# Performance work log

Hardware: AMD Instinct MI355X
Metric: run time of the kernel (lower is better)

Reference implementation:

```python
import jax, jax.numpy as jnp
import numpy as np

B, L, D, H, MEM, POL = 32, 256, 768, 12, 384, 3
DK = D // H
ALPHA, BETA, GAMA = 1.0, 0.25, 0.1


def _forward(sequence_output, pooled_output, adj_reshape, src_mask, aspect_mask,
             ln_g, ln_b, wq, bq, wk, bk, wd, bd, weight_m, bias_m,
             wa0, ba0, wa1, ba1, ws0, bs0, ws1, bs1, affine1, affine2, wc, bc):
    b, l, d = sequence_output.shape
    h = weight_m.shape[0]
    dk = d // h

    # custom LayerNorm (torch std is unbiased, ddof=1)
    mu = sequence_output.mean(-1, keepdims=True)
    sd = jnp.std(sequence_output, axis=-1, keepdims=True, ddof=1)
    x = ln_g * (sequence_output - mu) / (sd + 1e-6) + ln_b  # gcn_inputs (dropout = eval identity)

    aspect_outs = x * aspect_mask[:, :, None]

    # multi-head projections  [B,H,L,dk]
    q = (x @ wq + bq).reshape(b, l, h, dk).transpose(0, 2, 1, 3)
    k = (x @ wk + bk).reshape(b, l, h, dk).transpose(0, 2, 1, 3)
    asp = aspect_outs @ wd + bd                       # [B,L,dk]
    asp = jnp.broadcast_to(asp[:, None], (b, h, l, dk))

    # aspect-conditioned scores: tanh(aspect @ W_m @ K^T + b_m)   [B,H,L,L]
    asps = jnp.tanh(jnp.einsum('bhld,hde,bhme->bhlm', asp, weight_m, k) + bias_m[0])
    avg = asps.sum(axis=-2) / l                       # [B,H,L]

    # fusion overwrite: for each aspect index idx, row idx and col idx <- avg.
    # Sequential loop semantics (ascending idx, row-then-col) collapse to:
    #   both aspect (i,j): value = avg[min(i,j)];  row-only: avg[j];  col-only: avg[i]
    is_asp = aspect_mask > 0                          # [B,L]
    rowm = is_asp[:, None, :, None]
    colm = is_asp[:, None, None, :]
    avg_i = avg[..., :, None]                         # [B,H,L,1]
    avg_j = avg[..., None, :]                         # [B,H,1,L]
    ge = (jnp.arange(l)[:, None] >= jnp.arange(l)[None, :])  # i>=j -> min=j
    both_val = jnp.where(ge, avg_j, avg_i)
    aspect_scores = jnp.where(rowm & colm, both_val,
                      jnp.where(rowm, avg_j,
                        jnp.where(colm, avg_i, asps)))

    # standard scaled-dot attention
    scores = jnp.einsum('bhld,bhmd->bhlm', q, k) / jnp.sqrt(jnp.float32(dk))
    scores = jnp.where(src_mask[:, None, None, :] == 0, -1e9, scores)
    s_attn = jax.nn.softmax(scores, axis=-1)          # dropout = eval identity

    aspect_score_avg = aspect_scores.mean(axis=1)     # [B,L,L]
    adj_s = s_attn.mean(axis=1)                       # [B,L,L]

    eye = jnp.eye(l, dtype=adj_s.dtype)
    adj_s = adj_s * (1.0 - eye) + eye                 # zero diag then add identity
    adj_s = src_mask[:, :, None] * adj_s

    adj_r = jnp.exp(ALPHA * adj_reshape)
    dist_mask = aspect_score_avg > BETA
    adj_r = jnp.where(dist_mask, 1.0, adj_r)
    adj_ag = adj_r * aspect_score_avg

    log_p = jax.nn.log_softmax(adj_ag, axis=-1)
    log_q = jax.nn.log_softmax(adj_s, axis=-1)
    q_t = jnp.exp(log_q)
    kl = jnp.sum(q_t * (log_q - log_p))
    kl_loss = jnp.exp(-1.0 * kl * GAMA)

    denom_s = adj_s.sum(axis=2, keepdims=True) + 1.0
    denom_ag = adj_ag.sum(axis=2, keepdims=True) + 1.0

    out_ag, out_s = x, x
    was = [(wa0, ba0), (wa1, ba1)]
    wss = [(ws0, bs0), (ws1, bs1)]
    for li in range(2):
        g_ag = jax.nn.relu(((adj_ag @ out_ag) @ was[li][0] + was[li][1]) / denom_ag)
        g_s = jax.nn.relu(((adj_s @ out_s) @ wss[li][0] + wss[li][1]) / denom_s)
        A1 = jax.nn.softmax(jnp.einsum('bld,de,bme->blm', g_ag, affine1, g_s), axis=-1)
        A2 = jax.nn.softmax(jnp.einsum('bld,de,bme->blm', g_s, affine2, g_ag), axis=-1)
        out_ag = A1 @ g_s
        out_s = A2 @ g_ag   # gcn_drop = eval identity

    asp_wn = aspect_mask.sum(axis=1, keepdims=True)   # [B,1]
    m = aspect_mask[:, :, None]
    outputs1 = (out_ag * m).sum(axis=1) / asp_wn      # [B,MEM]
    outputs2 = (out_s * m).sum(axis=1) / asp_wn

    final = jnp.concatenate([outputs1, outputs2, pooled_output], axis=-1) @ wc + bc
    return final, kl_loss


def setup_inputs() -> dict:
    key = jax.random.key(0)
    ks = jax.random.split(key, 16)
    s = 0.02
    pos = jnp.arange(L)
    start = 5 + (jnp.arange(B) % 16)
    aspect_mask = ((pos[None, :] >= start[:, None]) & (pos[None, :] < start[:, None] + 3)).astype(jnp.float32)
    f32 = jnp.float32
    return {
        'sequence_output': jax.random.normal(ks[0], (B, L, D), f32),
        'pooled_output': jax.random.normal(ks[1], (B, D), f32),
        'adj_reshape': jax.random.uniform(ks[2], (B, L, L), f32),
        'src_mask': jnp.ones((B, L), f32),
        'aspect_mask': aspect_mask,
        'ln_g': jnp.ones((D,), f32), 'ln_b': jnp.zeros((D,), f32),
        'wq': jax.random.normal(ks[3], (D, D), f32) * s, 'bq': jnp.zeros((D,), f32),
        'wk': jax.random.normal(ks[4], (D, D), f32) * s, 'bk': jnp.zeros((D,), f32),
        'wd': jax.random.normal(ks[5], (D, DK), f32) * s, 'bd': jnp.zeros((DK,), f32),
        'weight_m': jax.random.normal(ks[6], (H, DK, DK), f32) * s,
        'bias_m': jnp.zeros((1,), f32),
        'wa0': jax.random.normal(ks[7], (D, MEM), f32) * s, 'ba0': jnp.zeros((MEM,), f32),
        'wa1': jax.random.normal(ks[8], (MEM, MEM), f32) * s, 'ba1': jnp.zeros((MEM,), f32),
        'ws0': jax.random.normal(ks[9], (D, MEM), f32) * s, 'bs0': jnp.zeros((MEM,), f32),
        'ws1': jax.random.normal(ks[10], (MEM, MEM), f32) * s, 'bs1': jnp.zeros((MEM,), f32),
        'affine1': jax.random.normal(ks[11], (MEM, MEM), f32) * s,
        'affine2': jax.random.normal(ks[12], (MEM, MEM), f32) * s,
        'wc': jax.random.normal(ks[13], (2 * D, POL), f32) * s, 'bc': jnp.zeros((POL,), f32),
    }


def reference(sequence_output, pooled_output, adj_reshape, src_mask, aspect_mask,
              ln_g, ln_b, wq, bq, wk, bk, wd, bd, weight_m, bias_m,
              wa0, ba0, wa1, ba1, ws0, bs0, ws1, bs1, affine1, affine2, wc, bc):
    return _forward(sequence_output, pooled_output, adj_reshape, src_mask, aspect_mask,
                    ln_g, ln_b, wq, bq, wk, bk, wd, bd, weight_m, bias_m,
                    wa0, ba0, wa1, ba1, ws0, bs0, ws1, bs1, affine1, affine2, wc, bc)
```

## Files before the change

### kernel.cpp

```cpp
#include <hip/hip_runtime.h>

#define B_ 32
#define L_ 256
#define D_ 768
#define H_ 12
#define DK_ 64
#define MEM_ 384

typedef __attribute__((ext_vector_type(8))) short bfrag8;
typedef __attribute__((ext_vector_type(8))) unsigned short us8;
typedef __attribute__((ext_vector_type(4))) float f32x4;

__device__ inline unsigned short f2bf(float f) {
  unsigned u = __float_as_uint(f);
  return (unsigned short)((u + 0x7fffu + ((u >> 16) & 1u)) >> 16);
}
__device__ inline float bf2f(unsigned short u) {
  return __uint_as_float(((unsigned)u) << 16);
}
__device__ inline float tanh_fast(float x) {
  x = fminf(fmaxf(x, -30.f), 30.f);
  float e = __expf(2.f * x);
  return (e - 1.f) * __builtin_amdgcn_rcpf(e + 1.f);
}
__device__ inline void gload_lds16(const unsigned short* g, unsigned short* l) {
  __builtin_amdgcn_global_load_lds(
      (__attribute__((address_space(1))) void*)(g),
      (__attribute__((address_space(3))) void*)(l), 16, 0, 0);
}

__device__ inline float waveRedSum(float v) {
#pragma unroll
  for (int o = 32; o; o >>= 1) v += __shfl_xor(v, o, 64);
  return v;
}
__device__ inline float waveRedMax(float v) {
#pragma unroll
  for (int o = 32; o; o >>= 1) v = fmaxf(v, __shfl_xor(v, o, 64));
  return v;
}
__device__ inline float blkRedSum(float v, float* red) {
  v = waveRedSum(v);
  int w = threadIdx.x >> 6;
  __syncthreads();
  if ((threadIdx.x & 63) == 0) red[w] = v;
  __syncthreads();
  return red[0] + red[1] + red[2] + red[3];
}
__device__ inline float blkRedMax(float v, float* red) {
  v = waveRedMax(v);
  int w = threadIdx.x >> 6;
  __syncthreads();
  if ((threadIdx.x & 63) == 0) red[w] = v;
  __syncthreads();
  return fmaxf(fmaxf(red[0], red[1]), fmaxf(red[2], red[3]));
}

__global__ __launch_bounds__(256) void prep_kernel(
    const float* __restrict__ seq, const float* __restrict__ lng,
    const float* __restrict__ lnb, float* __restrict__ xout,
    unsigned short* __restrict__ xbf,
    const float* __restrict__ wq, unsigned short* __restrict__ wqT,
    const float* __restrict__ wk, unsigned short* __restrict__ wkT,
    const float* __restrict__ wa0, unsigned short* __restrict__ wa0T,
    const float* __restrict__ ws0, unsigned short* __restrict__ ws0T,
    const float* __restrict__ wa1, unsigned short* __restrict__ wa1T,
    const float* __restrict__ ws1, unsigned short* __restrict__ ws1T,
    const float* __restrict__ aff1, unsigned short* __restrict__ aff1T,
    const float* __restrict__ aff2, unsigned short* __restrict__ aff2T,
    const float* __restrict__ wd, unsigned short* __restrict__ wdT,
    const float* __restrict__ wm, unsigned short* __restrict__ wmT) {
  int bid = blockIdx.x;
  if (bid >= 600) {
    long row = bid - 600;
    const float* p = seq + row * D_;
    float v[3];
#pragma unroll
    for (int i = 0; i < 3; ++i) v[i] = p[threadIdx.x + i * 256];
    __shared__ float red[4];
    float s = v[0] + v[1] + v[2];
    s = blkRedSum(s, red);
    float mu = s * (1.f / D_);
    float ss = 0.f;
#pragma unroll
    for (int i = 0; i < 3; ++i) { float d = v[i] - mu; ss += d * d; }
    ss = blkRedSum(ss, red);
    float sd = sqrtf(ss * (1.f / (D_ - 1)));
    float inv = 1.f / (sd + 1e-6f);
#pragma unroll
    for (int i = 0; i < 3; ++i) {
      int c = threadIdx.x + i * 256;
      float o = lng[c] * (v[i] - mu) * inv + lnb[c];
      xout[row * D_ + c] = o;
      xbf[row * D_ + c] = f2bf(o);
    }
    return;
  }
  const float* src; unsigned short* dst; int Rr, Cc, tIdx;
  if (bid < 144)      { src = wq;   dst = wqT;   Rr = 768; Cc = 768; tIdx = bid; }
  else if (bid < 288) { src = wk;   dst = wkT;   Rr = 768; Cc = 768; tIdx = bid - 144; }
  else if (bid < 360) { src = wa0;  dst = wa0T;  Rr = 768; Cc = 384; tIdx = bid - 288; }
  else if (bid < 432) { src = ws0;  dst = ws0T;  Rr = 768; Cc = 384; tIdx = bid - 360; }
  else if (bid < 468) { src = wa1;  dst = wa1T;  Rr = 384; Cc = 384; tIdx = bid - 432; }
  else if (bid < 504) { src = ws1;  dst = ws1T;  Rr = 384; Cc = 384; tIdx = bid - 468; }
  else if (bid < 540) { src = aff1; dst = aff1T; Rr = 384; Cc = 384; tIdx = bid - 504; }
  else if (bid < 576) { src = aff2; dst = aff2T; Rr = 384; Cc = 384; tIdx = bid - 540; }
  else if (bid < 588) { src = wd;   dst = wdT;   Rr = 768; Cc = 64;  tIdx = bid - 576; }
  else { int h = bid - 588; src = wm + h * 4096; dst = wmT + h * 4096; Rr = 64; Cc = 64; tIdx = 0; }
  __shared__ float tile[64][65];
  int nx = Cc >> 6;
  int c0 = (tIdx % nx) * 64, r0 = (tIdx / nx) * 64;
  int tx = threadIdx.x & 63, ty = threadIdx.x >> 6;
#pragma unroll
  for (int i = 0; i < 16; ++i)
    tile[ty + i * 4][tx] = src[(long)(r0 + ty + i * 4) * Cc + c0 + tx];
  __syncthreads();
#pragma unroll
  for (int i = 0; i < 16; ++i)
    dst[(long)(c0 + ty + i * 4) * Rr + r0 + tx] = f2bf(tile[tx][ty + i * 4]);
}

template <int MR>
__global__ __launch_bounds__(256) void gemm_bb(
    const unsigned short* __restrict__ A, const unsigned short* __restrict__ Bt,
    float* __restrict__ C, unsigned short* __restrict__ Cbf,
    unsigned short* __restrict__ CT,
    int M, int N, int K, long sA, long sB, long sC, long sCT,
    const float* __restrict__ bias, const float* __restrict__ rowDiv, int relu,
    const unsigned short* __restrict__ A2, const unsigned short* __restrict__ Bt2,
    float* __restrict__ C2, unsigned short* __restrict__ Cbf2,
    unsigned short* __restrict__ CT2,
    const float* __restrict__ bias2, const float* __restrict__ rowDiv2, int zsplit) {
  constexpr int MFRAG = MR / 32;
  constexpr int RW = MR / 2;
  constexpr int ASH = MR * 32;
  constexpr int BUFS = ASH + 4096;
  constexpr int TSH = 64 * (MR + 8);
  constexpr int SMN = (2 * BUFS > TSH) ? 2 * BUFS : TSH;
  __shared__ alignas(16) unsigned short smem[SMN];
  const int tid = threadIdx.x;
  const int bn = blockIdx.x, bm = blockIdx.y;
  int bz = blockIdx.z;
  const unsigned short* Ap = A; const unsigned short* Btp = Bt;
  float* Cp = C; unsigned short* Cbp = Cbf; unsigned short* CTp = CT;
  const float* biasp = bias; const float* rowDivp = rowDiv;
  if (zsplit > 0 && bz >= zsplit) {
    bz -= zsplit;
    Ap = A2; Btp = Bt2; Cp = C2; Cbp = Cbf2; CTp = CT2; biasp = bias2; rowDivp = rowDiv2;
  }
  Ap += (long)bz * sA; Btp += (long)bz * sB;
  if (Cp) Cp += (long)bz * sC;
  if (Cbp) Cbp += (long)bz * sC;
  if (CTp) CTp += (long)bz * sCT;

  f32x4 acc[MFRAG][4] = {};
  const int l = tid & 63, w = tid >> 6;
  const int wr = w >> 1, wc = w & 1;
  const int lr = l & 15, sg = l >> 4;

  const int rc = l >> 2;
  const int sslot = (l & 3) ^ ((rc >> 1) & 3);
  const unsigned short* gA0 = Ap + (long)(bm * MR + w * 16 + rc) * K + sslot * 8;
  const unsigned short* gA1 = (MR == 128)
      ? Ap + (long)(bm * MR + (w + 4) * 16 + rc) * K + sslot * 8 : nullptr;
  const unsigned short* gB0 = Btp + (long)(bn * 128 + w * 16 + rc) * K + sslot * 8;
  const unsigned short* gB1 = Btp + (long)(bn * 128 + (w + 4) * 16 + rc) * K + sslot * 8;
  const int stA0 = w * 512, stA1 = (w + 4) * 512;
  const int stB0 = ASH + w * 512, stB1 = ASH + (w + 4) * 512;

  const int swz = (sg ^ ((lr >> 1) & 3)) * 8;
  int aoff[MFRAG], boff[4];
#pragma unroll
  for (int m = 0; m < MFRAG; ++m) aoff[m] = (wr * RW + m * 16 + lr) * 32 + swz;
#pragma unroll
  for (int n = 0; n < 4; ++n) boff[n] = ASH + (wc * 64 + n * 16 + lr) * 32 + swz;

  const int nt = K >> 5;
  gload_lds16(gA0, smem + stA0);
  if (MR == 128) gload_lds16(gA1, smem + stA1);
  gload_lds16(gB0, smem + stB0);
  gload_lds16(gB1, smem + stB1);
  __syncthreads();

  for (int t = 0; t < nt; ++t) {
    const int cur = (t & 1) * BUFS;
    if (t + 1 < nt) {
      const int nxt = ((t + 1) & 1) * BUFS;
      const int k1 = (t + 1) << 5;
      gload_lds16(gA0 + k1, smem + nxt + stA0);
      if (MR == 128) gload_lds16(gA1 + k1, smem + nxt + stA1);
      gload_lds16(gB0 + k1, smem + nxt + stB0);
      gload_lds16(gB1 + k1, smem + nxt + stB1);
    }
    bfrag8 af[MFRAG], bf[4];
#pragma unroll
    for (int m = 0; m < MFRAG; ++m) af[m] = *(const bfrag8*)(smem + cur + aoff[m]);
#pragma unroll
    for (int n = 0; n < 4; ++n) bf[n] = *(const bfrag8*)(smem + cur + boff[n]);
#pragma unroll
    for (int m = 0; m < MFRAG; ++m)
#pragma unroll
      for (int n = 0; n < 4; ++n)
        acc[m][n] = __builtin_amdgcn_mfma_f32_16x16x32_bf16(af[m], bf[n], acc[m][n], 0, 0, 0);
    __syncthreads();
  }

  if (Cp || Cbp) {
#pragma unroll
    for (int m = 0; m < MFRAG; ++m) {
#pragma unroll
      for (int r = 0; r < 4; ++r) {
        int row = bm * MR + wr * RW + m * 16 + (l >> 4) * 4 + r;
        float rd = rowDivp ? 1.f / rowDivp[(long)bz * M + row] : 1.f;
#pragma unroll
        for (int n = 0; n < 4; ++n) {
          int col = bn * 128 + wc * 64 + n * 16 + lr;
          float v = acc[m][n][r];
          if (biasp) v += biasp[col];
          v *= rd;
          if (relu) v = fmaxf(v, 0.f);
          if (Cp) Cp[(long)row * N + col] = v;
          if (Cbp) Cbp[(long)row * N + col] = f2bf(v);
        }
      }
    }
  }
  if (CT) {
    auto Ts = (unsigned short(*)[MR + 8])smem;
#pragma unroll
    for (int ch = 0; ch < 2; ++ch) {
      __syncthreads();
      if (wc == ch) {
#pragma unroll
        for (int m = 0; m < MFRAG; ++m) {
#pragma unroll
          for (int r = 0; r < 4; ++r) {
            int rowl = wr * RW + m * 16 + (l >> 4) * 4 + r;
            float rd = rowDivp ? 1.f / rowDivp[(long)bz * M + bm * MR + rowl] : 1.f;
#pragma unroll
            for (int n = 0; n < 4; ++n) {
              int col = bn * 128 + wc * 64 + n * 16 + lr;
              float v = acc[m][n][r];
              if (biasp) v += biasp[col];
              v *= rd;
              if (relu) v = fmaxf(v, 0.f);
              Ts[n * 16 + lr][rowl] = f2bf(v);
            }
          }
        }
      }
      __syncthreads();
      int trow = tid >> 2, tc = (tid & 3) * (MR / 4);
      int colg = bn * 128 + ch * 64 + trow;
      int rowg = bm * MR + tc;
      unsigned short* dp = CTp + (long)(rowg >> 8) * sCT + (long)colg * 256 + (rowg & 255);
#pragma unroll
      for (int j = 0; j < MR / 32; ++j)
        *(us8*)(dp + j * 8) = *(const us8*)&Ts[trow][tc + j * 8];
    }
  }
}

__global__ __launch_bounds__(256) void attn_asp(
    const unsigned short* __restrict__ qbf, const unsigned short* __restrict__ kbf,
    const float* __restrict__ srcm, float* __restrict__ adj_s,
    unsigned short* __restrict__ adjsbf,
    const unsigned short* __restrict__ xbf, const unsigned short* __restrict__ wdT,
    const float* __restrict__ amask, const float* __restrict__ bd,
    unsigned short* __restrict__ aspbf) {
  int t = threadIdx.x;
  int w = t >> 6, l = t & 63;
  int lr = l & 15, kg = (l >> 4) * 8;
  if (blockIdx.x >= 512) {
    int l0 = (blockIdx.x - 512) << 4;
    const unsigned short* ap = xbf + (long)(l0 + lr) * D_ + kg;
    const unsigned short* bp = wdT + (long)(w * 16 + lr) * D_ + kg;
    f32x4 acc = {};
#pragma unroll
    for (int k0 = 0; k0 < D_; k0 += 32) {
      bfrag8 af = *(const bfrag8*)(ap + k0);
      bfrag8 bf = *(const bfrag8*)(bp + k0);
      acc = __builtin_amdgcn_mfma_f32_16x16x32_bf16(af, bf, acc, 0, 0, 0);
    }
    int col = w * 16 + lr;
#pragma unroll
    for (int r = 0; r < 4; ++r) {
      int row = l0 + (l >> 4) * 4 + r;
      float v = acc[r] * amask[row] + bd[col];
      aspbf[(long)row * DK_ + col] = f2bf(v);
    }
    return;
  }
  int blk = blockIdx.x;
  int b = blk >> 4, l0 = (blk & 15) << 4;
  int rbase = (l >> 4) * 4;
  __shared__ float red[6][2][16][8];
  float acc[4][4] = {};
  float cmv[4];
#pragma unroll
  for (int ct = 0; ct < 4; ++ct) cmv[ct] = srcm[b * L_ + w * 64 + ct * 16 + lr];

#pragma unroll 1
  for (int hp = 0; hp < 6; ++hp) {
    const unsigned short* ap = qbf + ((long)b * L_ + l0 + lr) * D_ + hp * 128 + kg;
    bfrag8 a00 = *(const bfrag8*)ap;
    bfrag8 a01 = *(const bfrag8*)(ap + 32);
    bfrag8 a10 = *(const bfrag8*)(ap + 64);
    bfrag8 a11 = *(const bfrag8*)(ap + 96);
    bfrag8 kv[4][4];
#pragma unroll
    for (int ct = 0; ct < 4; ++ct) {
      const unsigned short* bp =
          kbf + ((long)b * L_ + w * 64 + ct * 16 + lr) * D_ + hp * 128 + kg;
      kv[ct][0] = *(const bfrag8*)bp;
      kv[ct][1] = *(const bfrag8*)(bp + 32);
      kv[ct][2] = *(const bfrag8*)(bp + 64);
      kv[ct][3] = *(const bfrag8*)(bp + 96);
    }
    float sv0[4][4], sv1[4][4];
#pragma unroll
    for (int ct = 0; ct < 4; ++ct) {
      f32x4 c0 = {}, c1 = {};
      c0 = __builtin_amdgcn_mfma_f32_16x16x32_bf16(a00, kv[ct][0], c0, 0, 0, 0);
      c0 = __builtin_amdgcn_mfma_f32_16x16x32_bf16(a01, kv[ct][1], c0, 0, 0, 0);
      c1 = __builtin_amdgcn_mfma_f32_16x16x32_bf16(a10, kv[ct][2], c1, 0, 0, 0);
      c1 = __builtin_amdgcn_mfma_f32_16x16x32_bf16(a11, kv[ct][3], c1, 0, 0, 0);
      bool msk = (cmv[ct] == 0.f);
#pragma unroll
      for (int r = 0; r < 4; ++r) {
        sv0[ct][r] = msk ? -1e9f : c0[r] * 0.125f;
        sv1[ct][r] = msk ? -1e9f : c1[r] * 0.125f;
      }
    }
    float mx0a[4], mx1a[4];
#pragma unroll
    for (int r = 0; r < 4; ++r) {
      float m0 = fmaxf(fmaxf(sv0[0][r], sv0[1][r]), fmaxf(sv0[2][r], sv0[3][r]));
      float m1 = fmaxf(fmaxf(sv1[0][r], sv1[1][r]), fmaxf(sv1[2][r], sv1[3][r]));
#pragma unroll
      for (int o = 1; o < 16; o <<= 1) {
        m0 = fmaxf(m0, __shfl_xor(m0, o, 64));
        m1 = fmaxf(m1, __shfl_xor(m1, o, 64));
      }
      mx0a[r] = m0; mx1a[r] = m1;
      float s0 = 0.f, s1 = 0.f;
#pragma unroll
      for (int ct = 0; ct < 4; ++ct) {
        float e0 = __expf(sv0[ct][r] - m0);
        float e1 = __expf(sv1[ct][r] - m1);
        sv0[ct][r] = e0; sv1[ct][r] = e1;
        s0 += e0; s1 += e1;
      }
#pragma unroll
      for (int o = 1; o < 16; o <<= 1) {
        s0 += __shfl_xor(s0, o, 64);
        s1 += __shfl_xor(s1, o, 64);
      }
      if (lr == 0) {
        red[hp][0][rbase + r][w] = m0;
        red[hp][0][rbase + r][4 + w] = s0;
        red[hp][1][rbase + r][w] = m1;
        red[hp][1][rbase + r][4 + w] = s1;
      }
    }
    __syncthreads();
#pragma unroll
    for (int r = 0; r < 4; ++r) {
      f32x4 m4 = *(const f32x4*)&red[hp][0][rbase + r][0];
      f32x4 s4 = *(const f32x4*)&red[hp][0][rbase + r][4];
      float mt = fmaxf(fmaxf(m4[0], m4[1]), fmaxf(m4[2], m4[3]));
      float tot = s4[0] * __expf(m4[0] - mt) + s4[1] * __expf(m4[1] - mt) +
                  s4[2] * __expf(m4[2] - mt) + s4[3] * __expf(m4[3] - mt);
      float sc0 = __expf(mx0a[r] - mt) * __builtin_amdgcn_rcpf(tot);
      f32x4 n4 = *(const f32x4*)&red[hp][1][rbase + r][0];
      f32x4 t4 = *(const f32x4*)&red[hp][1][rbase + r][4];
      float nt = fmaxf(fmaxf(n4[0], n4[1]), fmaxf(n4[2], n4[3]));
      float tt = t4[0] * __expf(n4[0] - nt) + t4[1] * __expf(n4[1] - nt) +
                 t4[2] * __expf(n4[2] - nt) + t4[3] * __expf(n4[3] - nt);
      float sc1 = __expf(mx1a[r] - nt) * __builtin_amdgcn_rcpf(tt);
#pragma unroll
      for (int ct = 0; ct < 4; ++ct)
        acc[ct][r] += sv0[ct][r] * sc0 + sv1[ct][r] * sc1;
    }
  }

#pragma unroll
  for (int r = 0; r < 4; ++r) {
    int row = l0 + rbase + r;
    float rm = srcm[b * L_ + row];
#pragma unroll
    for (int ct = 0; ct < 4; ++ct) {
      int col = w * 64 + ct * 16 + lr;
      float v = acc[ct][r] * (1.f / H_);
      if (col == row) v = 1.f;
      v *= rm;
      long idx = ((long)b * L_ + row) * L_ + col;
      adj_s[idx] = v;
      adjsbf[idx] = f2bf(v);
    }
  }
}

__global__ __launch_bounds__(256) void asp_wm_v2(const unsigned short* __restrict__ aspbf,
                                                 const unsigned short* __restrict__ wmT,
                                                 unsigned short* __restrict__ tmpA) {
  int bh = blockIdx.x;
  int b = bh / H_, h = bh % H_;
  int t = threadIdx.x;
  int w = t >> 6, l = t & 63;
  int lr = l & 15, kg = (l >> 4) * 8;
  const unsigned short* wp = wmT + h * 4096;
  f32x4 acc[4][4] = {};
#pragma unroll
  for (int ks = 0; ks < 2; ++ks) {
    int k0 = ks * 32;
    bfrag8 af[4], bf[4];
#pragma unroll
    for (int m = 0; m < 4; ++m)
      af[m] = *(const bfrag8*)(aspbf + (long)(b * L_ + w * 64 + m * 16 + lr) * DK_ + k0 + kg);
#pragma unroll
    for (int n = 0; n < 4; ++n)
      bf[n] = *(const bfrag8*)(wp + (n * 16 + lr) * 64 + k0 + kg);
#pragma unroll
    for (int m = 0; m < 4; ++m)
#pragma unroll
      for (int n = 0; n < 4; ++n)
        acc[m][n] = __builtin_amdgcn_mfma_f32_16x16x32_bf16(af[m], bf[n], acc[m][n], 0, 0, 0);
  }
#pragma unroll
  for (int m = 0; m < 4; ++m)
#pragma unroll
    for (int n = 0; n < 4; ++n)
#pragma unroll
      for (int r = 0; r < 4; ++r) {
        int row = w * 64 + m * 16 + (l >> 4) * 4 + r;
        int col = n * 16 + lr;
        tmpA[(((long)b * H_ + h) * L_ + row) * DK_ + col] = f2bf(acc[m][n][r]);
      }
}

__global__ __launch_bounds__(256) void gemm_sfmx(
    const unsigned short* __restrict__ u1, const unsigned short* __restrict__ g1,
    unsigned short* __restrict__ P1,
    const unsigned short* __restrict__ u2, const unsigned short* __restrict__ g2,
    unsigned short* __restrict__ P2) {
  int bm = blockIdx.x;
  int bz = blockIdx.y;
  const unsigned short* Ap; const unsigned short* Bp; unsigned short* Pp;
  if (bz < 32) {
    Ap = u1 + (long)bz * L_ * MEM_; Bp = g1 + (long)bz * L_ * MEM_;
    Pp = P1 + (long)bz * L_ * L_;
  } else {
    int z = bz - 32;
    Ap = u2 + (long)z * L_ * MEM_; Bp = g2 + (long)z * L_ * MEM_;
    Pp = P2 + (long)z * L_ * L_;
  }
  __shared__ unsigned short As[64][40];
  __shared__ unsigned short Bs[256][40];
  __shared__ float redm[2][64];
  __shared__ float reds[2][64];
  const int t = threadIdx.x;
  const int l = t & 63, w = t >> 6;
  const int wr = w >> 1, wc = w & 1;
  const int lr = l & 15, kg = (l >> 4) * 8;
  f32x4 acc[2][8] = {};
  const int arA = t >> 2, akA = (t & 3) * 8;

  for (int k0 = 0; k0 < MEM_; k0 += 32) {
    *(us8*)&As[arA][akA] = *(const us8*)(Ap + (long)(bm * 64 + arA) * MEM_ + k0 + akA);
#pragma unroll
    for (int j = 0; j < 4; ++j)
      *(us8*)&Bs[t][j * 8] = *(const us8*)(Bp + (long)t * MEM_ + k0 + j * 8);
    __syncthreads();
    bfrag8 af[2], bf[8];
#pragma unroll
    for (int m = 0; m < 2; ++m) af[m] = *(const bfrag8*)&As[wr * 32 + m * 16 + lr][kg];
#pragma unroll
    for (int n = 0; n < 8; ++n) bf[n] = *(const bfrag8*)&Bs[wc * 128 + n * 16 + lr][kg];
#pragma unroll
    for (int m = 0; m < 2; ++m)
#pragma unroll
      for (int n = 0; n < 8; ++n)
        acc[m][n] = __builtin_amdgcn_mfma_f32_16x16x32_bf16(af[m], bf[n], acc[m][n], 0, 0, 0);
    __syncthreads();
  }

#pragma unroll
  for (int m = 0; m < 2; ++m) {
#pragma unroll
    for (int r = 0; r < 4; ++r) {
      int lrow = wr * 32 + m * 16 + (l >> 4) * 4 + r;
      float mx = -1e30f;
#pragma unroll
      for (int n = 0; n < 8; ++n) mx = fmaxf(mx, acc[m][n][r]);
#pragma unroll
      for (int o = 1; o < 16; o <<= 1) mx = fmaxf(mx, __shfl_xor(mx, o, 64));
      if (lr == 0) redm[wc][lrow] = mx;
    }
  }
  __syncthreads();
#pragma unroll
  for (int m = 0; m < 2; ++m) {
#pragma unroll
    for (int r = 0; r < 4; ++r) {
      int lrow = wr * 32 + m * 16 + (l >> 4) * 4 + r;
      float mx = fmaxf(redm[0][lrow], redm[1][lrow]);
      float s = 0.f;
#pragma unroll
      for (int n = 0; n < 8; ++n) {
        float e = __expf(acc[m][n][r] - mx);
        acc[m][n][r] = e;
        s += e;
      }
#pragma unroll
      for (int o = 1; o < 16; o <<= 1) s += __shfl_xor(s, o, 64);
      if (lr == 0) reds[wc][lrow] = s;
    }
  }
  __syncthreads();
#pragma unroll
  for (int m = 0; m < 2; ++m) {
#pragma unroll
    for (int r = 0; r < 4; ++r) {
      int lrow = wr * 32 + m * 16 + (l >> 4) * 4 + r;
      float inv = 1.f / (reds[0][lrow] + reds[1][lrow]);
      int row = bm * 64 + lrow;
#pragma unroll
      for (int n = 0; n < 8; ++n) {
        int col = wc * 128 + n * 16 + lr;
        Pp[(long)row * L_ + col] = f2bf(acc[m][n][r] * inv);
      }
    }
  }
}

__global__ __launch_bounds__(256) void asps_mean_v2(
    const unsigned short* __restrict__ tmpA,
    const unsigned short* __restrict__ kbf,
    const float* __restrict__ bias_m,
    float* __restrict__ asps_mean) {
  int blk = blockIdx.x;
  int b = blk >> 4, l0 = (blk & 15) << 4;
  int t = threadIdx.x;
  int w = t >> 6, l = t & 63;
  int lr = l & 15, kg = (l >> 4) * 8;
  float bm = bias_m[0];
  float accg[4][4] = {};
  for (int h = 0; h < H_; ++h) {
    const unsigned short* ap = tmpA + (((long)b * H_ + h) * L_ + l0 + lr) * 64 + kg;
    bfrag8 af0 = *(const bfrag8*)ap;
    bfrag8 af1 = *(const bfrag8*)(ap + 32);
#pragma unroll
    for (int ct = 0; ct < 4; ++ct) {
      const unsigned short* bp =
          kbf + ((long)b * L_ + w * 64 + ct * 16 + lr) * D_ + h * 64 + kg;
      bfrag8 bf0 = *(const bfrag8*)bp;
      bfrag8 bf1 = *(const bfrag8*)(bp + 32);
      f32x4 accl = {};
      accl = __builtin_amdgcn_mfma_f32_16x16x32_bf16(af0, bf0, accl, 0, 0, 0);
      accl = __builtin_amdgcn_mfma_f32_16x16x32_bf16(af1, bf1, accl, 0, 0, 0);
#pragma unroll
      for (int r = 0; r < 4; ++r) accg[ct][r] += tanh_fast(accl[r] + bm);
    }
  }
#pragma unroll
  for (int ct = 0; ct < 4; ++ct) {
    int col = w * 64 + ct * 16 + lr;
#pragma unroll
    for (int r = 0; r < 4; ++r) {
      int row = l0 + (l >> 4) * 4 + r;
      asps_mean[((long)b * L_ + row) * L_ + col] = accg[ct][r] * (1.f / H_);
    }
  }
}

__global__ __launch_bounds__(1024) void avgh_kernel(const float* __restrict__ asps_mean,
                                                    float* __restrict__ avgH) {
  int b = blockIdx.x;
  int m = threadIdx.x & 255, q = threadIdx.x >> 8;
  __shared__ float part[4][256];
  float s = 0.f;
  for (int l = q * 64; l < q * 64 + 64; ++l)
    s += asps_mean[((long)b * L_ + l) * L_ + m];
  part[q][m] = s;
  __syncthreads();
  if (q == 0)
    avgH[b * L_ + m] = (part[0][m] + part[1][m] + part[2][m] + part[3][m]) * (1.f / L_);
}

__global__ __launch_bounds__(256) void adjag_kl(const float* __restrict__ asps_mean,
                                                const float* __restrict__ avgH,
                                                const float* __restrict__ amask,
                                                const float* __restrict__ adjr,
                                                const float* __restrict__ adj_s,
                                                float* __restrict__ adj_ag,
                                                unsigned short* __restrict__ adjagbf,
                                                float* __restrict__ klpart,
                                                float* __restrict__ den_s,
                                                float* __restrict__ den_ag) {
  long row = blockIdx.x;
  int m = threadIdx.x;
  int l = (int)(row & 255);
  int b = (int)(row >> 8);
  long idx = row * L_ + m;
  bool rowa = amask[b * L_ + l] > 0.f;
  bool cola = amask[b * L_ + m] > 0.f;
  float asa;
  if (rowa && cola) asa = (l >= m) ? avgH[b * L_ + m] : avgH[b * L_ + l];
  else if (rowa)    asa = avgH[b * L_ + m];
  else if (cola)    asa = avgH[b * L_ + l];
  else              asa = asps_mean[idx];
  float r = (asa > 0.25f) ? 1.f : expf(adjr[idx]);
  float a = r * asa;
  adj_ag[idx] = a;
  adjagbf[idx] = f2bf(a);

  __shared__ float red[4];
  float s = adj_s[idx];
  float sum_s = blkRedSum(s, red);
  float sum_a = blkRedSum(a, red);
  float mx_s = blkRedMax(s, red);
  float mx_a = blkRedMax(a, red);
  float es = expf(s - mx_s), ea = expf(a - mx_a);
  float ses = blkRedSum(es, red);
  float sea = blkRedSum(ea, red);
  float logq = (s - mx_s) - logf(ses);
  float logp = (a - mx_a) - logf(sea);
  float term = (es / ses) * (logq - logp);
  float kp = blkRedSum(term, red);
  if (m == 0) {
    klpart[row] = kp;
    den_s[row] = sum_s + 1.f;
    den_ag[row] = sum_a + 1.f;
  }
}

__global__ __launch_bounds__(256) void final_kernel(const unsigned short* __restrict__ o_ag,
                                                    const unsigned short* __restrict__ o_s,
                                                    const float* __restrict__ pooled,
                                                    const float* __restrict__ amask,
                                                    const float* __restrict__ wc,
                                                    const float* __restrict__ bc,
                                                    const float* __restrict__ klpart,
                                                    float* __restrict__ dout) {
  int b = blockIdx.x, t = threadIdx.x;
  __shared__ float red[4];
  if (b == B_) {
    float s = 0.f;
    for (int i = t; i < B_ * L_; i += 256) s += klpart[i];
    s = blkRedSum(s, red);
    if (t == 0) dout[96] = expf(-s * 0.1f);
    return;
  }
  __shared__ float cS[1536];
  __shared__ float maskS[256];
  maskS[t] = amask[b * L_ + t];
  float wn = blkRedSum(maskS[t], red);
  for (int e = t; e < MEM_; e += 256) {
    float s1 = 0.f, s2 = 0.f;
    for (int l = 0; l < L_; ++l) {
      float mk = maskS[l];
      if (mk != 0.f) {
        s1 += mk * bf2f(o_ag[((long)b * L_ + l) * MEM_ + e]);
        s2 += mk * bf2f(o_s[((long)b * L_ + l) * MEM_ + e]);
      }
    }
    cS[e] = s1 / wn;
    cS[MEM_ + e] = s2 / wn;
  }
  for (int j = t; j < D_; j += 256) cS[2 * MEM_ + j] = pooled[b * D_ + j];
  __syncthreads();
  float p0 = 0.f, p1 = 0.f, p2 = 0.f;
  for (int j = t; j < 1536; j += 256) {
    float v = cS[j];
    p0 += v * wc[j * 3 + 0];
    p1 += v * wc[j * 3 + 1];
    p2 += v * wc[j * 3 + 2];
  }
  p0 = blkRedSum(p0, red);
  p1 = blkRedSum(p1, red);
  p2 = blkRedSum(p2, red);
  if (t == 0) {
    dout[b * 3 + 0] = p0 + bc[0];
    dout[b * 3 + 1] = p1 + bc[1];
    dout[b * 3 + 2] = p2 + bc[2];
  }
}

extern "C" void kernel_launch(void* const* d_in, const int* in_sizes, int n_in,
                              void* d_out, int out_size, void* d_ws, size_t ws_size,
                              hipStream_t stream) {
  const float* seq    = (const float*)d_in[0];
  const float* pooled = (const float*)d_in[1];
  const float* adjr   = (const float*)d_in[2];
  const float* srcm   = (const float*)d_in[3];
  const float* amask  = (const float*)d_in[4];
  const float* ln_g   = (const float*)d_in[5];
  const float* ln_b   = (const float*)d_in[6];
  const float* wq     = (const float*)d_in[7];
  const float* bq     = (const float*)d_in[8];
  const float* wk     = (const float*)d_in[9];
  const float* bk     = (const float*)d_in[10];
  const float* wd     = (const float*)d_in[11];
  const float* bd     = (const float*)d_in[12];
  const float* wm     = (const float*)d_in[13];
  const float* bm     = (const float*)d_in[14];
  const float* wa0    = (const float*)d_in[15];
  const float* ba0    = (const float*)d_in[16];
  const float* wa1    = (const float*)d_in[17];
  const float* ba1    = (const float*)d_in[18];
  const float* ws0    = (const float*)d_in[19];
  const float* bs0    = (const float*)d_in[20];
  const float* ws1    = (const float*)d_in[21];
  const float* bs1    = (const float*)d_in[22];
  const float* aff1   = (const float*)d_in[23];
  const float* aff2   = (const float*)d_in[24];
  const float* wc     = (const float*)d_in[25];
  const float* bc     = (const float*)d_in[26];

  float* ws = (float*)d_ws;
  float* S0 = ws;
  float* S1 = S0 + 6291456;
  float* S2 = S1 + 3145728;
  float* S3 = S2 + 3145728;
  float* S4 = S3 + 3145728;
  float* S5 = S4 + 524288;
  float* adj_s  = S5 + 2097152;
  float* adj_ag = adj_s + 2097152;
  unsigned short* adjsbf  = (unsigned short*)(adj_ag + 2097152);
  unsigned short* adjagbf = adjsbf + 2097152;
  unsigned short* wT      = adjagbf + 2097152;
  unsigned short* wqT   = wT;
  unsigned short* wkT   = wT + 589824;
  unsigned short* wa0T  = wT + 1179648;
  unsigned short* ws0T  = wT + 1474560;
  unsigned short* wa1T  = wT + 1769472;
  unsigned short* ws1T  = wT + 1916928;
  unsigned short* aff1T = wT + 2064384;
  unsigned short* aff2T = wT + 2211840;
  float* tail   = (float*)(wT + 2359296);
  float* avgH   = tail;
  float* den_s  = avgH + 8192;
  float* den_ag = den_s + 8192;
  float* klp    = den_ag + 8192;

  float* x = S0;
  unsigned short* o_agbf = (unsigned short*)S0;
  unsigned short* o_sbf  = o_agbf + 3145728;
  unsigned short* gTag   = o_agbf + 6291456;
  unsigned short* gTs    = o_agbf + 9437184;
  unsigned short* xbf    = (unsigned short*)S1;
  unsigned short* qbf    = (unsigned short*)S2;
  unsigned short* tmpA   = (unsigned short*)S2;
  unsigned short* g_agbf = (unsigned short*)S2;
  unsigned short* g_sbf  = g_agbf + 3145728;
  unsigned short* kbf    = (unsigned short*)S3;
  unsigned short* tTag   = (unsigned short*)S3;
  unsigned short* tTs    = tTag + 3145728;
  unsigned short* u1bf   = (unsigned short*)S3;
  unsigned short* u2bf   = u1bf + 3145728;
  unsigned short* aspbf  = (unsigned short*)S4;
  unsigned short* wdT    = aspbf + 524288;
  unsigned short* wmT    = wdT + 49152;
  float* asps = S5;
  unsigned short* P1bf = (unsigned short*)S5;
  unsigned short* P2bf = P1bf + 2097152;
  float* dout = (float*)d_out;

  const long sAdjSh = (long)L_ * L_;
  const long sMemSh = (long)L_ * MEM_;

  prep_kernel<<<600 + B_ * L_, 256, 0, stream>>>(
      seq, ln_g, ln_b, x, xbf, wq, wqT, wk, wkT, wa0, wa0T, ws0, ws0T,
      wa1, wa1T, ws1, ws1T, aff1, aff1T, aff2, aff2T, wd, wdT, wm, wmT);
  gemm_bb<128><<<dim3(6, 64, 2), 256, 0, stream>>>(
      xbf, wqT, nullptr, qbf, nullptr, 8192, 768, 768, 0, 0, 0, 0, bq, nullptr, 0,
      xbf, wkT, nullptr, kbf, nullptr, bk, nullptr, 1);
  attn_asp<<<1024, 256, 0, stream>>>(qbf, kbf, srcm, adj_s, adjsbf,
                                     xbf, wdT, amask, bd, aspbf);
  asp_wm_v2<<<B_ * H_, 256, 0, stream>>>(aspbf, wmT, tmpA);
  asps_mean_v2<<<B_ * 16, 256, 0, stream>>>(tmpA, kbf, bm, asps);
  avgh_kernel<<<B_, 1024, 0, stream>>>(asps, avgH);
  adjag_kl<<<B_ * L_, 256, 0, stream>>>(asps, avgH, amask, adjr, adj_s,
                                        adj_ag, adjagbf, klp, den_s, den_ag);

  for (int li = 0; li < 2; ++li) {
    int Kd = li ? MEM_ : D_;
    const unsigned short* inag = li ? o_agbf : xbf;
    const unsigned short* ins  = li ? o_sbf : xbf;
    const unsigned short* wAT = li ? wa1T : wa0T;
    const float* bA = li ? ba1 : ba0;
    const unsigned short* wST = li ? ws1T : ws0T;
    const float* bS = li ? bs1 : bs0;
    gemm_bb<64><<<dim3(3, 128, 2), 256, 0, stream>>>(
        inag, wAT, nullptr, nullptr, tTag, 8192, MEM_, Kd, 0, 0, 0, sMemSh,
        nullptr, nullptr, 0,
        ins, wST, nullptr, nullptr, tTs, nullptr, nullptr, 1);
    gemm_bb<64><<<dim3(3, 4, 64), 256, 0, stream>>>(
        adjagbf, tTag, nullptr, g_agbf, gTag, L_, MEM_, L_, sAdjSh, sMemSh, sMemSh,
        sMemSh, bA, den_ag, 1,
        adjsbf, tTs, nullptr, g_sbf, gTs, bS, den_s, 32);
    gemm_bb<64><<<dim3(3, 128, 2), 256, 0, stream>>>(
        g_agbf, aff1T, nullptr, u1bf, nullptr, 8192, MEM_, MEM_, 0, 0, 0, 0,
        nullptr, nullptr, 0,
        g_sbf, aff2T, nullptr, u2bf, nullptr, nullptr, nullptr, 1);
    gemm_sfmx<<<dim3(4, 64), 256, 0, stream>>>(u1bf, g_sbf, P1bf, u2bf, g_agbf, P2bf);
    gemm_bb<64><<<dim3(3, 4, 64), 256, 0, stream>>>(
        P1bf, gTs, nullptr, o_agbf, nullptr, L_, MEM_, L_, sAdjSh, sMemSh, sMemSh, 0,
        nullptr, nullptr, 0,
        P2bf, gTag, nullptr, o_sbf, nullptr, nullptr, nullptr, 32);
  }

  final_kernel<<<B_ + 1, 256, 0, stream>>>(o_agbf, o_sbf, pooled, amask, wc, bc,
                                           klp, dout);
}
```

Before: 408.0 us.

## Split attention heads across two blocks, defer adj_s finalize, async double-buffer gemm_sfmx

The attention kernel now splits the six head-pairs across two blocks per row tile, doubling the grid. Each block writes fp32 partial sums, and the blocks are interleaved so that neighbouring blocks work on different batches. The diagonal, mask and bf16 conversion of adj_s move into adjag_kl, which sums the two partials there, and the unused fp32 adj_s and adj_ag stores are dropped. gemm_sfmx switches to direct global-to-LDS loads into swizzled, double-buffered shared memory so the next tile's loads overlap the current tile's MFMAs. In exchange, the extra fp32 partial buffers add write and read traffic.

```diff
diff --git a/kernel.cpp b/kernel.cpp
--- a/kernel.cpp
+++ b/kernel.cpp
@@ -263,16 +263,16 @@
 
 __global__ __launch_bounds__(256) void attn_asp(
     const unsigned short* __restrict__ qbf, const unsigned short* __restrict__ kbf,
-    const float* __restrict__ srcm, float* __restrict__ adj_s,
-    unsigned short* __restrict__ adjsbf,
+    const float* __restrict__ srcm,
+    float* __restrict__ part0, float* __restrict__ part1,
     const unsigned short* __restrict__ xbf, const unsigned short* __restrict__ wdT,
     const float* __restrict__ amask, const float* __restrict__ bd,
     unsigned short* __restrict__ aspbf) {
   int t = threadIdx.x;
   int w = t >> 6, l = t & 63;
   int lr = l & 15, kg = (l >> 4) * 8;
-  if (blockIdx.x >= 512) {
-    int l0 = (blockIdx.x - 512) << 4;
+  if (blockIdx.x >= 1024) {
+    int l0 = (blockIdx.x - 1024) << 4;
     const unsigned short* ap = xbf + (long)(l0 + lr) * D_ + kg;
     const unsigned short* bp = wdT + (long)(w * 16 + lr) * D_ + kg;
     f32x4 acc = {};
@@ -291,17 +291,21 @@
     }
     return;
   }
-  int blk = blockIdx.x;
-  int b = blk >> 4, l0 = (blk & 15) << 4;
+  int d = blockIdx.x;
+  int b = (d & 7) + 8 * ((d >> 3) & 3);
+  int rest = d >> 5;
+  int l0 = (rest & 15) << 4;
+  int half = rest >> 4;
   int rbase = (l >> 4) * 4;
-  __shared__ float red[6][2][16][8];
+  __shared__ float red[3][2][16][8];
   float acc[4][4] = {};
   float cmv[4];
 #pragma unroll
   for (int ct = 0; ct < 4; ++ct) cmv[ct] = srcm[b * L_ + w * 64 + ct * 16 + lr];
 
 #pragma unroll 1
-  for (int hp = 0; hp < 6; ++hp) {
+  for (int ph = 0; ph < 3; ++ph) {
+    int hp = half * 3 + ph;
     const unsigned short* ap = qbf + ((long)b * L_ + l0 + lr) * D_ + hp * 128 + kg;
     bfrag8 a00 = *(const bfrag8*)ap;
     bfrag8 a01 = *(const bfrag8*)(ap + 32);
@@ -357,23 +361,23 @@
         s1 += __shfl_xor(s1, o, 64);
       }
       if (lr == 0) {
-        red[hp][0][rbase + r][w] = m0;
-        red[hp][0][rbase + r][4 + w] = s0;
-        red[hp][1][rbase + r][w] = m1;
-        red[hp][1][rbase + r][4 + w] = s1;
+        red[ph][0][rbase + r][w] = m0;
+        red[ph][0][rbase + r][4 + w] = s0;
+        red[ph][1][rbase + r][w] = m1;
+        red[ph][1][rbase + r][4 + w] = s1;
       }
     }
     __syncthreads();
 #pragma unroll
     for (int r = 0; r < 4; ++r) {
-      f32x4 m4 = *(const f32x4*)&red[hp][0][rbase + r][0];
-      f32x4 s4 = *(const f32x4*)&red[hp][0][rbase + r][4];
+      f32x4 m4 = *(const f32x4*)&red[ph][0][rbase + r][0];
+      f32x4 s4 = *(const f32x4*)&red[ph][0][rbase + r][4];
       float mt = fmaxf(fmaxf(m4[0], m4[1]), fmaxf(m4[2], m4[3]));
       float tot = s4[0] * __expf(m4[0] - mt) + s4[1] * __expf(m4[1] - mt) +
                   s4[2] * __expf(m4[2] - mt) + s4[3] * __expf(m4[3] - mt);
       float sc0 = __expf(mx0a[r] - mt) * __builtin_amdgcn_rcpf(tot);
-      f32x4 n4 = *(const f32x4*)&red[hp][1][rbase + r][0];
-      f32x4 t4 = *(const f32x4*)&red[hp][1][rbase + r][4];
+      f32x4 n4 = *(const f32x4*)&red[ph][1][rbase + r][0];
+      f32x4 t4 = *(const f32x4*)&red[ph][1][rbase + r][4];
       float nt = fmaxf(fmaxf(n4[0], n4[1]), fmaxf(n4[2], n4[3]));
       float tt = t4[0] * __expf(n4[0] - nt) + t4[1] * __expf(n4[1] - nt) +
                  t4[2] * __expf(n4[2] - nt) + t4[3] * __expf(n4[3] - nt);
@@ -384,19 +388,14 @@
     }
   }
 
+  float* pp = half ? part1 : part0;
 #pragma unroll
   for (int r = 0; r < 4; ++r) {
     int row = l0 + rbase + r;
-    float rm = srcm[b * L_ + row];
 #pragma unroll
     for (int ct = 0; ct < 4; ++ct) {
       int col = w * 64 + ct * 16 + lr;
-      float v = acc[ct][r] * (1.f / H_);
-      if (col == row) v = 1.f;
-      v *= rm;
-      long idx = ((long)b * L_ + row) * L_ + col;
-      adj_s[idx] = v;
-      adjsbf[idx] = f2bf(v);
+      pp[((long)b * L_ + row) * L_ + col] = acc[ct][r];
     }
   }
 }
@@ -444,6 +443,11 @@
     unsigned short* __restrict__ P1,
     const unsigned short* __restrict__ u2, const unsigned short* __restrict__ g2,
     unsigned short* __restrict__ P2) {
+  constexpr int ASH = 64 * 32;
+  constexpr int BUFS = ASH + 8192;
+  __shared__ alignas(16) unsigned short smem[2 * BUFS];
+  __shared__ float redm[2][64];
+  __shared__ float reds[2][64];
   int bm = blockIdx.x;
   int bz = blockIdx.y;
   const unsigned short* Ap; const unsigned short* Bp; unsigned short* Pp;
@@ -455,28 +459,51 @@
     Ap = u2 + (long)z * L_ * MEM_; Bp = g2 + (long)z * L_ * MEM_;
     Pp = P2 + (long)z * L_ * L_;
   }
-  __shared__ unsigned short As[64][40];
-  __shared__ unsigned short Bs[256][40];
-  __shared__ float redm[2][64];
-  __shared__ float reds[2][64];
   const int t = threadIdx.x;
   const int l = t & 63, w = t >> 6;
   const int wr = w >> 1, wc = w & 1;
-  const int lr = l & 15, kg = (l >> 4) * 8;
+  const int lr = l & 15, sg = l >> 4;
   f32x4 acc[2][8] = {};
-  const int arA = t >> 2, akA = (t & 3) * 8;
-
-  for (int k0 = 0; k0 < MEM_; k0 += 32) {
-    *(us8*)&As[arA][akA] = *(const us8*)(Ap + (long)(bm * 64 + arA) * MEM_ + k0 + akA);
-#pragma unroll
-    for (int j = 0; j < 4; ++j)
-      *(us8*)&Bs[t][j * 8] = *(const us8*)(Bp + (long)t * MEM_ + k0 + j * 8);
-    __syncthreads();
+
+  const int rc = l >> 2;
+  const int sslot = (l & 3) ^ ((rc >> 1) & 3);
+  const unsigned short* gA = Ap + (long)(bm * 64 + w * 16 + rc) * MEM_ + sslot * 8;
+  const unsigned short* gB[4];
+#pragma unroll
+  for (int j = 0; j < 4; ++j)
+    gB[j] = Bp + (long)(w * 64 + j * 16 + rc) * MEM_ + sslot * 8;
+  const int stA = w * 512;
+  int stB[4];
+#pragma unroll
+  for (int j = 0; j < 4; ++j) stB[j] = ASH + (w * 4 + j) * 512;
+
+  const int swz = (sg ^ ((lr >> 1) & 3)) * 8;
+  int aoff[2], boff[8];
+#pragma unroll
+  for (int m = 0; m < 2; ++m) aoff[m] = (wr * 32 + m * 16 + lr) * 32 + swz;
+#pragma unroll
+  for (int n = 0; n < 8; ++n) boff[n] = ASH + (wc * 128 + n * 16 + lr) * 32 + swz;
+
+  gload_lds16(gA, smem + stA);
+#pragma unroll
+  for (int j = 0; j < 4; ++j) gload_lds16(gB[j], smem + stB[j]);
+  __syncthreads();
+
+  constexpr int NT = MEM_ / 32;
+  for (int tt = 0; tt < NT; ++tt) {
+    const int cur = (tt & 1) * BUFS;
+    if (tt + 1 < NT) {
+      const int nxt = ((tt + 1) & 1) * BUFS;
+      const int k1 = (tt + 1) << 5;
+      gload_lds16(gA + k1, smem + nxt + stA);
+#pragma unroll
+      for (int j = 0; j < 4; ++j) gload_lds16(gB[j] + k1, smem + nxt + stB[j]);
+    }
     bfrag8 af[2], bf[8];
 #pragma unroll
-    for (int m = 0; m < 2; ++m) af[m] = *(const bfrag8*)&As[wr * 32 + m * 16 + lr][kg];
-#pragma unroll
-    for (int n = 0; n < 8; ++n) bf[n] = *(const bfrag8*)&Bs[wc * 128 + n * 16 + lr][kg];
+    for (int m = 0; m < 2; ++m) af[m] = *(const bfrag8*)(smem + cur + aoff[m]);
+#pragma unroll
+    for (int n = 0; n < 8; ++n) bf[n] = *(const bfrag8*)(smem + cur + boff[n]);
 #pragma unroll
     for (int m = 0; m < 2; ++m)
 #pragma unroll
@@ -588,12 +615,14 @@
     avgH[b * L_ + m] = (part[0][m] + part[1][m] + part[2][m] + part[3][m]) * (1.f / L_);
 }
 
-__global__ __launch_bounds__(256) void adjag_kl(const float* __restrict__ asps_mean,
+__global__ __launch_bounds__(256) void adjag_kl(const float* __restrict__ part0,
+                                                const float* __restrict__ part1,
+                                                const float* __restrict__ srcm,
+                                                const float* __restrict__ asps_mean,
                                                 const float* __restrict__ avgH,
                                                 const float* __restrict__ amask,
                                                 const float* __restrict__ adjr,
-                                                const float* __restrict__ adj_s,
-                                                float* __restrict__ adj_ag,
+                                                unsigned short* __restrict__ adjsbf,
                                                 unsigned short* __restrict__ adjagbf,
                                                 float* __restrict__ klpart,
                                                 float* __restrict__ den_s,
@@ -603,6 +632,10 @@
   int l = (int)(row & 255);
   int b = (int)(row >> 8);
   long idx = row * L_ + m;
+  float s = (part0[idx] + part1[idx]) * (1.f / H_);
+  if (m == l) s = 1.f;
+  s *= srcm[b * L_ + l];
+  adjsbf[idx] = f2bf(s);
   bool rowa = amask[b * L_ + l] > 0.f;
   bool cola = amask[b * L_ + m] > 0.f;
   float asa;
@@ -612,11 +645,9 @@
   else              asa = asps_mean[idx];
   float r = (asa > 0.25f) ? 1.f : expf(adjr[idx]);
   float a = r * asa;
-  adj_ag[idx] = a;
   adjagbf[idx] = f2bf(a);
 
   __shared__ float red[4];
-  float s = adj_s[idx];
   float sum_s = blkRedSum(s, red);
   float sum_a = blkRedSum(a, red);
   float mx_s = blkRedMax(s, red);
@@ -725,9 +756,9 @@
   float* S3 = S2 + 3145728;
   float* S4 = S3 + 3145728;
   float* S5 = S4 + 524288;
-  float* adj_s  = S5 + 2097152;
-  float* adj_ag = adj_s + 2097152;
-  unsigned short* adjsbf  = (unsigned short*)(adj_ag + 2097152);
+  float* part0  = S5 + 2097152;
+  float* part1  = part0 + 2097152;
+  unsigned short* adjsbf  = (unsigned short*)(part1 + 2097152);
   unsigned short* adjagbf = adjsbf + 2097152;
   unsigned short* wT      = adjagbf + 2097152;
   unsigned short* wqT   = wT;
@@ -776,13 +807,13 @@
   gemm_bb<128><<<dim3(6, 64, 2), 256, 0, stream>>>(
       xbf, wqT, nullptr, qbf, nullptr, 8192, 768, 768, 0, 0, 0, 0, bq, nullptr, 0,
       xbf, wkT, nullptr, kbf, nullptr, bk, nullptr, 1);
-  attn_asp<<<1024, 256, 0, stream>>>(qbf, kbf, srcm, adj_s, adjsbf,
+  attn_asp<<<1536, 256, 0, stream>>>(qbf, kbf, srcm, part0, part1,
                                      xbf, wdT, amask, bd, aspbf);
   asp_wm_v2<<<B_ * H_, 256, 0, stream>>>(aspbf, wmT, tmpA);
   asps_mean_v2<<<B_ * 16, 256, 0, stream>>>(tmpA, kbf, bm, asps);
   avgh_kernel<<<B_, 1024, 0, stream>>>(asps, avgH);
-  adjag_kl<<<B_ * L_, 256, 0, stream>>>(asps, avgH, amask, adjr, adj_s,
-                                        adj_ag, adjagbf, klp, den_s, den_ag);
+  adjag_kl<<<B_ * L_, 256, 0, stream>>>(part0, part1, srcm, asps, avgH, amask, adjr,
+                                        adjsbf, adjagbf, klp, den_s, den_ag);
 
   for (int li = 0; li < 2; ++li) {
     int Kd = li ? MEM_ : D_;
```

After: 395.2 us. -3.1%, faster.
